# Optimization experiments

Measured on AMD Instinct MI355X. Metric: run time of the kernel, lower is better.

The kernel has to match this reference:

```python
import jax, jax.numpy as jnp
import numpy as np

B, F, D = 4096, 39, 128          # batch, num_fields, embed_dim
FIELD_DIM = 10000                # per-field vocab (uniform)
K_SPACE = [1, 256, 512]
M_SPACE = [1, 2, 4]
THRESHOLD = 500
NUM = F                          # prior_flag all ones -> num == field_len
# pairs (j, m) actually used by forward: (0,0) plus all (j>=1, m)
PAIRS = [(0, 0)] + [(j, m) for j in range(1, len(K_SPACE)) for m in range(len(M_SPACE))]

def _rows(j, m):
    return NUM * THRESHOLD if j == 0 else NUM * K_SPACE[j]

def setup_inputs() -> dict:
    key = jax.random.key(0)
    ks = jax.random.split(key, 2 + 2 * len(PAIRS))
    inp = {
        "x": jax.random.randint(ks[0], (B, F), 0, FIELD_DIM),
        "arch_prob": jax.random.uniform(ks[1], (F, len(K_SPACE) * len(M_SPACE)), dtype=jnp.float32),
    }
    for n, (j, m) in enumerate(PAIRS):
        rows = _rows(j, m)
        inp[f"cb_{j}_{m}"] = jax.random.normal(ks[2 + 2 * n], (rows, D), dtype=jnp.float32)
        inp[f"idx_{j}_{m}"] = jax.random.randint(ks[3 + 2 * n], (F * FIELD_DIM, M_SPACE[m]), 0, rows)
    return inp

def reference(x, arch_prob, cb_0_0, idx_0_0, cb_1_0, idx_1_0, cb_1_1, idx_1_1,
              cb_1_2, idx_1_2, cb_2_0, idx_2_0, cb_2_1, idx_2_1, cb_2_2, idx_2_2):
    cbs = {(0, 0): cb_0_0, (1, 0): cb_1_0, (1, 1): cb_1_1, (1, 2): cb_1_2,
           (2, 0): cb_2_0, (2, 1): cb_2_1, (2, 2): cb_2_2}
    idxs = {(0, 0): idx_0_0, (1, 0): idx_1_0, (1, 1): idx_1_1, (1, 2): idx_1_2,
            (2, 0): idx_2_0, (2, 1): idx_2_1, (2, 2): idx_2_2}
    offsets = (FIELD_DIM * jnp.arange(F)).astype(x.dtype)   # offsets_a
    xg = x + offsets[None, :]                               # (B, F) global feature ids
    nM = len(M_SPACE)
    emb = jnp.zeros((B, F, D), dtype=jnp.float32)
    for (j, m) in PAIRS:                                    # small fixed set of 7 codebooks
        Mn = M_SPACE[m]
        plen = D // Mn
        idx = idxs[(j, m)][xg]                              # (B, F, Mn) codeword ids
        # original gathers the full row then slices [i*plen:(i+1)*plen] for subvector i;
        # reshape the codebook to (rows, Mn, plen) and gather only the needed slice.
        cb = cbs[(j, m)].reshape(-1, Mn, plen)
        gathered = cb[idx, jnp.arange(Mn)[None, None, :], :]  # (B, F, Mn, plen)
        scale = arch_prob[:, j * nM + m]                    # (F,) per-field arch weight
        emb = emb + (scale[None, :, None, None] * gathered).reshape(B, F, D)
    return emb
```

## Files before the change

### kernel.cpp

```cpp
#include <hip/hip_runtime.h>

#define BB 4096
#define FF 39
#define DD 128
#define FIELD_DIM 10000
#define NXCD 8

__global__ __launch_bounds__(256) void mixq_embed(
    const int* __restrict__ x,
    const float* __restrict__ arch_prob,
    const float* __restrict__ cb00, const int* __restrict__ i00,
    const float* __restrict__ cb10, const int* __restrict__ i10,
    const float* __restrict__ cb11, const int* __restrict__ i11,
    const float* __restrict__ cb12, const int* __restrict__ i12,
    const float* __restrict__ cb20, const int* __restrict__ i20,
    const float* __restrict__ cb21, const int* __restrict__ i21,
    const float* __restrict__ cb22, const int* __restrict__ i22,
    float* __restrict__ out)
{
    const int nwg  = gridDim.x;
    const int cpx  = nwg >> 3;
    const int orig = blockIdx.x;
    const int wgid = (orig & (NXCD - 1)) * cpx + (orig >> 3);

    const int tid  = wgid * 256 + (int)threadIdx.x;
    const int item = tid >> 5;
    const int lane = tid & 31;
    const int d0   = lane << 2;

    const int f = item >> 12;
    const int b = item & (BB - 1);

    const int xg = x[b * FF + f] + f * FIELD_DIM;
    const float* ap = arch_prob + f * 9;

    float4 acc = make_float4(0.f, 0.f, 0.f, 0.f);

#define DO_PAIR(cb, idx, M, col)                                              \
    do {                                                                      \
        const int plen = DD / (M);                                            \
        int k = (M) == 1 ? 0 : d0 / plen;                                     \
        int r = idx[(size_t)xg * (M) + k];                                    \
        float4 v = *reinterpret_cast<const float4*>((cb) + (size_t)r * DD + d0); \
        float s = ap[col];                                                    \
        acc.x += s * v.x;                                                     \
        acc.y += s * v.y;                                                     \
        acc.z += s * v.z;                                                     \
        acc.w += s * v.w;                                                     \
    } while (0)

    DO_PAIR(cb00, i00, 1, 0);
    DO_PAIR(cb10, i10, 1, 3);
    DO_PAIR(cb11, i11, 2, 4);
    DO_PAIR(cb12, i12, 4, 5);
    DO_PAIR(cb20, i20, 1, 6);
    DO_PAIR(cb21, i21, 2, 7);
    DO_PAIR(cb22, i22, 4, 8);
#undef DO_PAIR

    float* dst = out + ((size_t)b * FF + f) * DD + d0;
    __builtin_nontemporal_store(acc.x, dst + 0);
    __builtin_nontemporal_store(acc.y, dst + 1);
    __builtin_nontemporal_store(acc.z, dst + 2);
    __builtin_nontemporal_store(acc.w, dst + 3);
}

extern "C" void kernel_launch(void* const* d_in, const int* in_sizes, int n_in,
                              void* d_out, int out_size, void* d_ws, size_t ws_size,
                              hipStream_t stream) {
    const int*   x  = (const int*)d_in[0];
    const float* ap = (const float*)d_in[1];
    const float* cb00 = (const float*)d_in[2];
    const int*   i00  = (const int*)d_in[3];
    const float* cb10 = (const float*)d_in[4];
    const int*   i10  = (const int*)d_in[5];
    const float* cb11 = (const float*)d_in[6];
    const int*   i11  = (const int*)d_in[7];
    const float* cb12 = (const float*)d_in[8];
    const int*   i12  = (const int*)d_in[9];
    const float* cb20 = (const float*)d_in[10];
    const int*   i20  = (const int*)d_in[11];
    const float* cb21 = (const float*)d_in[12];
    const int*   i21  = (const int*)d_in[13];
    const float* cb22 = (const float*)d_in[14];
    const int*   i22  = (const int*)d_in[15];
    float* out = (float*)d_out;

    const long long total_threads = (long long)BB * FF * 32;
    const int threads = 256;
    const int blocks = (int)((total_threads + threads - 1) / threads);

    mixq_embed<<<blocks, threads, 0, stream>>>(
        x, ap, cb00, i00, cb10, i10, cb11, i11, cb12, i12,
        cb20, i20, cb21, i21, cb22, i22, out);
}
```

Measured before the change: 90.18 us.

## Split embedding halves across XCD groups and hoist all index loads

Remaps work so each XCD group handles one 64-float half of the embedding dimension, with 16 lanes per item instead of 32. Each half then only touches half of every codebook row's sub-vectors, which is meant to improve per-XCD L2 locality on the codebooks. All seven codeword index loads are hoisted ahead of the gathers to raise memory-level parallelism. In exchange, each item's x and index loads are now repeated across the two halves, and the mapping assumes the grid size is divisible by 8.

```diff
diff --git a/kernel.cpp b/kernel.cpp
--- a/kernel.cpp
+++ b/kernel.cpp
@@ -4,7 +4,6 @@
 #define FF 39
 #define DD 128
 #define FIELD_DIM 10000
-#define NXCD 8
 
 __global__ __launch_bounds__(256) void mixq_embed(
     const int* __restrict__ x,
@@ -19,46 +18,53 @@
     float* __restrict__ out)
 {
     const int nwg  = gridDim.x;
-    const int cpx  = nwg >> 3;
-    const int orig = blockIdx.x;
-    const int wgid = (orig & (NXCD - 1)) * cpx + (orig >> 3);
+    const int perx = nwg >> 3;
+    const int blk  = blockIdx.x;
+    const int xcd  = blk & 7;
+    const int h    = xcd >> 2;
+    const int wh   = (xcd & 3) * perx + (blk >> 3);
 
-    const int tid  = wgid * 256 + (int)threadIdx.x;
-    const int item = tid >> 5;
-    const int lane = tid & 31;
-    const int d0   = lane << 2;
+    const int t   = (int)threadIdx.x;
+    const int sub = (t >> 4) & 1;
+    const int li  = t & 15;
+    const int ii  = wh * 16 + ((t >> 5) << 1) + sub;
+    const int f   = ii >> 12;
+    const int bb  = ii & (BB - 1);
+    const int d0  = (h << 6) + (li << 2);
 
-    const int f = item >> 12;
-    const int b = item & (BB - 1);
+    const int xg = x[bb * FF + f] + f * FIELD_DIM;
+    const float* ap = arch_prob + f * 9;
 
-    const int xg = x[b * FF + f] + f * FIELD_DIM;
-    const float* ap = arch_prob + f * 9;
+    const int k4 = (h << 1) + (li >> 3);
+
+    int r00 = i00[xg];
+    int r10 = i10[xg];
+    int r11 = i11[(size_t)xg * 2 + h];
+    int r12 = i12[(size_t)xg * 4 + k4];
+    int r20 = i20[xg];
+    int r21 = i21[(size_t)xg * 2 + h];
+    int r22 = i22[(size_t)xg * 4 + k4];
 
     float4 acc = make_float4(0.f, 0.f, 0.f, 0.f);
 
-#define DO_PAIR(cb, idx, M, col)                                              \
+#define GATHER_FMA(cb, r, col)                                                \
     do {                                                                      \
-        const int plen = DD / (M);                                            \
-        int k = (M) == 1 ? 0 : d0 / plen;                                     \
-        int r = idx[(size_t)xg * (M) + k];                                    \
-        float4 v = *reinterpret_cast<const float4*>((cb) + (size_t)r * DD + d0); \
+        float4 v = *reinterpret_cast<const float4*>((cb) + (size_t)(r) * DD + d0); \
         float s = ap[col];                                                    \
-        acc.x += s * v.x;                                                     \
-        acc.y += s * v.y;                                                     \
-        acc.z += s * v.z;                                                     \
-        acc.w += s * v.w;                                                     \
+        acc.x += s * v.x; acc.y += s * v.y;                                   \
+        acc.z += s * v.z; acc.w += s * v.w;                                   \
     } while (0)
 
-    DO_PAIR(cb00, i00, 1, 0);
-    DO_PAIR(cb10, i10, 1, 3);
-    DO_PAIR(cb11, i11, 2, 4);
-    DO_PAIR(cb12, i12, 4, 5);
-    DO_PAIR(cb20, i20, 1, 6);
-    DO_PAIR(cb21, i21, 2, 7);
-    DO_PAIR(cb22, i22, 4, 8);
-#undef DO_PAIR
+    GATHER_FMA(cb00, r00, 0);
+    GATHER_FMA(cb10, r10, 3);
+    GATHER_FMA(cb11, r11, 4);
+    GATHER_FMA(cb12, r12, 5);
+    GATHER_FMA(cb20, r20, 6);
+    GATHER_FMA(cb21, r21, 7);
+    GATHER_FMA(cb22, r22, 8);
+#undef GATHER_FMA
 
-    float* dst = out + ((size_t)b * FF + f) * DD + d0;
+    float* dst = out + ((size_t)bb * FF + f) * DD + d0;
     __builtin_nontemporal_store(acc.x, dst + 0);
     __builtin_nontemporal_store(acc.y, dst + 1);
     __builtin_nontemporal_store(acc.z, dst + 2);
```

Result: faster. 88.06 us (-2.4%).
